# Kernel optimization log

Hardware: AMD Instinct MI355X
Metric: run time of the kernel (lower is better)

## Reference

```python
import jax, jax.numpy as jnp
import numpy as np

CHUNK_SIZE = 64
EPS = 1e-6


def setup_inputs() -> dict:
    key = jax.random.key(0)
    ks = jax.random.split(key, 5)
    B, NH, S, DH = 2, 16, 4096, 64
    return {
        "q": jax.random.normal(ks[0], (B, NH, S, DH), dtype=jnp.float32),
        "k": jax.random.normal(ks[1], (B, NH, S, DH), dtype=jnp.float32),
        "v": jax.random.normal(ks[2], (B, NH, S, DH), dtype=jnp.float32),
        "igate_preact": jax.random.normal(ks[3], (B, NH, S), dtype=jnp.float32),
        "fgate_preact": jax.random.normal(ks[4], (B, NH, S), dtype=jnp.float32),
    }


def _mlstm_intra(q, k, v, ig, fg, chunk_size, eps):
    # q,k,v: [B,NH,S,DH]; ig,fg: [B,NH,S]
    B, NH, S, DH = q.shape
    L = chunk_size
    NC = S // L
    qc = q.reshape(B, NH, NC, L, DH)
    kc = k.reshape(B, NH, NC, L, DH)
    vc = v.reshape(B, NH, NC, L, DH)
    igc = ig.reshape(B, NH, NC, L)
    fgc = fg.reshape(B, NH, NC, L)

    # log forget gates and their within-chunk cumulative sums
    log_fg = jax.nn.log_sigmoid(fgc)                      # [B,NH,NC,L]
    log_fg_cum = jnp.cumsum(log_fg, axis=-1)              # [B,NH,NC,L]

    # gated decay matrix: logD[i,j] = sum_{t=j+1..i} log f_t + i_j  for j<=i
    log_fg_mat = log_fg_cum[..., :, None] - log_fg_cum[..., None, :]  # [B,NH,NC,L,L]
    log_D = log_fg_mat + igc[..., None, :]
    causal = jnp.tril(jnp.ones((L, L), dtype=bool))
    log_D = jnp.where(causal, log_D, -jnp.inf)

    # stabilizer (row-wise max)
    m = jnp.max(log_D, axis=-1)                           # [B,NH,NC,L]
    D = jnp.exp(log_D - m[..., None])                     # [B,NH,NC,L,L]

    # QK scores scaled, gated by decay matrix
    scale = 1.0 / jnp.sqrt(jnp.asarray(DH, dtype=q.dtype))
    scores = jnp.einsum("bncld,bncsd->bncls", qc, kc) * scale
    C = scores * D                                        # [B,NH,NC,L,L]

    # stabilized normalizer: max(|row sum|, exp(-m))
    n = jnp.maximum(jnp.abs(jnp.sum(C, axis=-1)), jnp.exp(-m))  # [B,NH,NC,L]
    h = jnp.einsum("bncls,bncsd->bncld", C, vc) / (n[..., None] + eps)
    return h.reshape(B, NH, S, DH)


def reference(q, k, v, igate_preact, fgate_preact):
    return _mlstm_intra(q, k, v, igate_preact, fgate_preact, CHUNK_SIZE, EPS)
```

## Files before the change

### kernel.cpp

```cpp
#include <hip/hip_runtime.h>
#include <hip/hip_bf16.h>
#include <math.h>

namespace {

typedef __bf16 bf16x8 __attribute__((ext_vector_type(8)));
typedef float f32x4 __attribute__((ext_vector_type(4)));

constexpr int L = 64;
constexpr int DH = 64;

__device__ __forceinline__ int swz(int row, int col) {
  return row * 128 + (((col >> 3) ^ (row & 7)) << 4) + (col & 7) * 2;
}

__device__ __forceinline__ unsigned short bfbits(float f) {
  __bf16 h = (__bf16)f;
  return __builtin_bit_cast(unsigned short, h);
}
__device__ __forceinline__ __bf16 tobf(float f) { return (__bf16)f; }

__global__ __launch_bounds__(64) void mlstm_mfma(
    const float* __restrict__ q, const float* __restrict__ k,
    const float* __restrict__ v, const float* __restrict__ ig,
    const float* __restrict__ fg, float* __restrict__ out) {

  __shared__ __align__(16) char tile[64 * 128];
  __shared__ float ea_sh[64], eb_sh[64], em_sh[64];

  const int lane = threadIdx.x;
  const int m = lane & 15;
  const int g = lane >> 4;
  const size_t cbase = (size_t)blockIdx.x * (L * DH);
  const size_t gb = (size_t)blockIdx.x * L;

  const float fgv = fg[gb + lane];
  const float igv = ig[gb + lane];

  const float4* v4 = (const float4*)(v + cbase);
  float4 vbuf[16];
#pragma unroll
  for (int it = 0; it < 16; ++it) vbuf[it] = v4[it * 64 + lane];

  bf16x8 kf[4][2], qf[4][2];
#pragma unroll
  for (int rb = 0; rb < 4; ++rb)
#pragma unroll
    for (int kb = 0; kb < 2; ++kb) {
      const int off = (rb * 16 + m) * 64 + kb * 32 + g * 8;
      const float4 k0 = *(const float4*)(k + cbase + off);
      const float4 k1 = *(const float4*)(k + cbase + off + 4);
      const float4 q0 = *(const float4*)(q + cbase + off);
      const float4 q1 = *(const float4*)(q + cbase + off + 4);
      kf[rb][kb] = bf16x8{tobf(k0.x), tobf(k0.y), tobf(k0.z), tobf(k0.w),
                          tobf(k1.x), tobf(k1.y), tobf(k1.z), tobf(k1.w)};
      qf[rb][kb] = bf16x8{tobf(q0.x), tobf(q0.y), tobf(q0.z), tobf(q0.w),
                          tobf(q1.x), tobf(q1.y), tobf(q1.z), tobf(q1.w)};
    }

  {
    const float lf = fminf(fgv, 0.f) - log1pf(__expf(-fabsf(fgv)));
    float cum = lf;
#pragma unroll
    for (int o = 1; o < 64; o <<= 1) {
      const float t = __shfl_up(cum, o, 64);
      if (lane >= o) cum += t;
    }
    const float a = igv - cum;
    float b = a;
#pragma unroll
    for (int o = 1; o < 64; o <<= 1) {
      const float t = __shfl_up(b, o, 64);
      if (lane >= o) b = fmaxf(b, t);
    }
    const float bmax = __shfl(b, 63, 64);
    ea_sh[lane] = 0.125f * __expf(a - bmax);
    eb_sh[lane] = __expf(bmax - b);
    em_sh[lane] = __expf(-(b + cum));
  }

  {
    unsigned short* vt = (unsigned short*)tile;
#pragma unroll
    for (int it = 0; it < 16; ++it) {
      const int idx = it * 64 + lane;
      const int j = idx >> 4;
      const int d0 = (idx & 15) * 4;
      vt[swz(d0 + 0, j) >> 1] = bfbits(vbuf[it].x);
      vt[swz(d0 + 1, j) >> 1] = bfbits(vbuf[it].y);
      vt[swz(d0 + 2, j) >> 1] = bfbits(vbuf[it].z);
      vt[swz(d0 + 3, j) >> 1] = bfbits(vbuf[it].w);
    }
  }

  bf16x8 vfr[4][2];
#pragma unroll
  for (int db = 0; db < 4; ++db)
#pragma unroll
    for (int jb = 0; jb < 2; ++jb)
      vfr[db][jb] = *(const bf16x8*)(tile + swz(db * 16 + m, jb * 32 + g * 8));

  f32x4 st[4][4];
#pragma unroll
  for (int cb = 0; cb < 4; ++cb)
#pragma unroll
    for (int rb = 0; rb < 4; ++rb) {
      if (rb > cb) continue;
      f32x4 acc = {0.f, 0.f, 0.f, 0.f};
      acc = __builtin_amdgcn_mfma_f32_16x16x32_bf16(kf[rb][0], qf[cb][0], acc, 0, 0, 0);
      acc = __builtin_amdgcn_mfma_f32_16x16x32_bf16(kf[rb][1], qf[cb][1], acc, 0, 0, 0);
      st[rb][cb] = acc;
    }

  float ea_j[4][4];
#pragma unroll
  for (int rb = 0; rb < 4; ++rb)
#pragma unroll
    for (int e = 0; e < 4; ++e) ea_j[rb][e] = ea_sh[rb * 16 + g * 4 + e];

  float invr[4];
#pragma unroll
  for (int cb = 0; cb < 4; ++cb) {
    const int i = cb * 16 + m;
    const float ebv = eb_sh[i];
    float rs = 0.f;
#pragma unroll
    for (int rb = 0; rb < 4; ++rb) {
      unsigned long long wp = 0ull;
      if (rb <= cb) {
#pragma unroll
        for (int e = 0; e < 4; ++e) {
          const int j = rb * 16 + g * 4 + e;
          const float val = (j <= i) ? st[rb][cb][e] * ea_j[rb][e] * ebv : 0.f;
          rs += val;
          wp |= (unsigned long long)bfbits(val) << (16 * e);
        }
      }
      *(unsigned long long*)(tile + swz(i, rb * 16 + g * 4)) = wp;
    }
    rs += __shfl_xor(rs, 16, 64);
    rs += __shfl_xor(rs, 32, 64);
    const float n = fmaxf(fabsf(rs), em_sh[i]);
    invr[cb] = 1.f / (n + 1e-6f);
  }

#pragma unroll
  for (int ib = 0; ib < 4; ++ib) {
    const int i = ib * 16 + m;
    const bf16x8 c0 = *(const bf16x8*)(tile + swz(i, g * 8));
    f32x4 acc[4];
#pragma unroll
    for (int db = 0; db < 4; ++db) {
      f32x4 z = {0.f, 0.f, 0.f, 0.f};
      acc[db] = __builtin_amdgcn_mfma_f32_16x16x32_bf16(vfr[db][0], c0, z, 0, 0, 0);
    }
    if (ib >= 2) {
      const bf16x8 c1 = *(const bf16x8*)(tile + swz(i, 32 + g * 8));
#pragma unroll
      for (int db = 0; db < 4; ++db)
        acc[db] = __builtin_amdgcn_mfma_f32_16x16x32_bf16(vfr[db][1], c1, acc[db], 0, 0, 0);
    }
    const float iv = invr[ib];
    float* op = out + cbase + i * 64 + g * 4;
#pragma unroll
    for (int db = 0; db < 4; ++db) {
      const f32x4 hv = acc[db];
      *(float4*)(op + db * 16) =
          make_float4(hv[0] * iv, hv[1] * iv, hv[2] * iv, hv[3] * iv);
    }
  }
}

}

extern "C" void kernel_launch(void* const* d_in, const int* in_sizes, int n_in,
                              void* d_out, int out_size, void* d_ws,
                              size_t ws_size, hipStream_t stream) {
  const float* q = (const float*)d_in[0];
  const float* k = (const float*)d_in[1];
  const float* v = (const float*)d_in[2];
  const float* ig = (const float*)d_in[3];
  const float* fg = (const float*)d_in[4];
  float* out = (float*)d_out;

  const int total = in_sizes[0];
  const int nchunks = total / (L * DH);
  mlstm_mfma<<<dim3(nchunks), dim3(64), 0, stream>>>(q, k, v, ig, fg, out);
}
```

Measured before the change: 28.21 us.

## Split each chunk across four wavefronts, one per 16-row query block

Each chunk is now handled by a 256-thread block in which each wavefront owns one 16-row query block. It loads only the K blocks it needs under the causal mask and writes its C tile into a private LDS region. V is staged cooperatively, with a barrier so every wave can read the shared transposed V tile. The LDS swizzle key is also changed to reduce bank conflicts. The aim is more parallelism and latency hiding per chunk and shorter serial work per wave. The cost is a block-wide sync, some redundant K loads across waves, and load imbalance between the causal blocks.

```diff
diff --git a/kernel.cpp b/kernel.cpp
--- a/kernel.cpp
+++ b/kernel.cpp
@@ -10,8 +10,13 @@
 constexpr int L = 64;
 constexpr int DH = 64;
 
-__device__ __forceinline__ int swz(int row, int col) {
-  return row * 128 + (((col >> 3) ^ (row & 7)) << 4) + (col & 7) * 2;
+__device__ __forceinline__ int kkey(int r) { return (r ^ (r >> 2)) & 7; }
+
+__device__ __forceinline__ int swzV(int d, int j) {
+  return d * 128 + ((((j >> 3) ^ kkey(d)) & 7) << 4) + (j & 7) * 2;
+}
+__device__ __forceinline__ int swzC(int r, int j) {
+  return r * 128 + ((((j >> 3) ^ kkey(r)) & 7) << 4) + (j & 7) * 2;
 }
 
 __device__ __forceinline__ unsigned short bfbits(float f) {
@@ -20,45 +25,60 @@
 }
 __device__ __forceinline__ __bf16 tobf(float f) { return (__bf16)f; }
 
-__global__ __launch_bounds__(64) void mlstm_mfma(
+__global__ __launch_bounds__(256) void mlstm_mfma(
     const float* __restrict__ q, const float* __restrict__ k,
     const float* __restrict__ v, const float* __restrict__ ig,
     const float* __restrict__ fg, float* __restrict__ out) {
 
-  __shared__ __align__(16) char tile[64 * 128];
-  __shared__ float ea_sh[64], eb_sh[64], em_sh[64];
-
-  const int lane = threadIdx.x;
+  __shared__ __align__(16) char lds[8192 + 4 * 2048];
+  __shared__ __align__(16) float ea_sh[64];
+  __shared__ __align__(16) float eb_sh[64];
+  __shared__ __align__(16) float em_sh[64];
+
+  const int tid = threadIdx.x;
+  const int w = tid >> 6;
+  const int lane = tid & 63;
   const int m = lane & 15;
   const int g = lane >> 4;
   const size_t cbase = (size_t)blockIdx.x * (L * DH);
   const size_t gb = (size_t)blockIdx.x * L;
 
-  const float fgv = fg[gb + lane];
-  const float igv = ig[gb + lane];
-
   const float4* v4 = (const float4*)(v + cbase);
-  float4 vbuf[16];
-#pragma unroll
-  for (int it = 0; it < 16; ++it) vbuf[it] = v4[it * 64 + lane];
-
-  bf16x8 kf[4][2], qf[4][2];
-#pragma unroll
-  for (int rb = 0; rb < 4; ++rb)
-#pragma unroll
-    for (int kb = 0; kb < 2; ++kb) {
-      const int off = (rb * 16 + m) * 64 + kb * 32 + g * 8;
-      const float4 k0 = *(const float4*)(k + cbase + off);
-      const float4 k1 = *(const float4*)(k + cbase + off + 4);
-      const float4 q0 = *(const float4*)(q + cbase + off);
-      const float4 q1 = *(const float4*)(q + cbase + off + 4);
-      kf[rb][kb] = bf16x8{tobf(k0.x), tobf(k0.y), tobf(k0.z), tobf(k0.w),
-                          tobf(k1.x), tobf(k1.y), tobf(k1.z), tobf(k1.w)};
-      qf[rb][kb] = bf16x8{tobf(q0.x), tobf(q0.y), tobf(q0.z), tobf(q0.w),
-                          tobf(q1.x), tobf(q1.y), tobf(q1.z), tobf(q1.w)};
-    }
-
-  {
+  float4 vbuf[4];
+#pragma unroll
+  for (int it = 0; it < 4; ++it) vbuf[it] = v4[it * 256 + tid];
+
+  float fgv = 0.f, igv = 0.f;
+  if (w == 0) {
+    fgv = fg[gb + lane];
+    igv = ig[gb + lane];
+  }
+
+  bf16x8 qf[2];
+#pragma unroll
+  for (int kb = 0; kb < 2; ++kb) {
+    const int off = (w * 16 + m) * 64 + kb * 32 + g * 8;
+    const float4 q0 = *(const float4*)(q + cbase + off);
+    const float4 q1 = *(const float4*)(q + cbase + off + 4);
+    qf[kb] = bf16x8{tobf(q0.x), tobf(q0.y), tobf(q0.z), tobf(q0.w),
+                    tobf(q1.x), tobf(q1.y), tobf(q1.z), tobf(q1.w)};
+  }
+  bf16x8 kf[4][2];
+#pragma unroll
+  for (int rb = 0; rb < 4; ++rb) {
+    if (rb <= w) {
+#pragma unroll
+      for (int kb = 0; kb < 2; ++kb) {
+        const int off = (rb * 16 + m) * 64 + kb * 32 + g * 8;
+        const float4 k0 = *(const float4*)(k + cbase + off);
+        const float4 k1 = *(const float4*)(k + cbase + off + 4);
+        kf[rb][kb] = bf16x8{tobf(k0.x), tobf(k0.y), tobf(k0.z), tobf(k0.w),
+                            tobf(k1.x), tobf(k1.y), tobf(k1.z), tobf(k1.w)};
+      }
+    }
+  }
+
+  if (w == 0) {
     const float lf = fminf(fgv, 0.f) - log1pf(__expf(-fabsf(fgv)));
     float cum = lf;
 #pragma unroll
@@ -80,94 +100,89 @@
   }
 
   {
-    unsigned short* vt = (unsigned short*)tile;
-#pragma unroll
-    for (int it = 0; it < 16; ++it) {
-      const int idx = it * 64 + lane;
+    unsigned short* vt = (unsigned short*)lds;
+#pragma unroll
+    for (int it = 0; it < 4; ++it) {
+      const int idx = it * 256 + tid;
       const int j = idx >> 4;
       const int d0 = (idx & 15) * 4;
-      vt[swz(d0 + 0, j) >> 1] = bfbits(vbuf[it].x);
-      vt[swz(d0 + 1, j) >> 1] = bfbits(vbuf[it].y);
-      vt[swz(d0 + 2, j) >> 1] = bfbits(vbuf[it].z);
-      vt[swz(d0 + 3, j) >> 1] = bfbits(vbuf[it].w);
-    }
-  }
-
+      vt[swzV(d0 + 0, j) >> 1] = bfbits(vbuf[it].x);
+      vt[swzV(d0 + 1, j) >> 1] = bfbits(vbuf[it].y);
+      vt[swzV(d0 + 2, j) >> 1] = bfbits(vbuf[it].z);
+      vt[swzV(d0 + 3, j) >> 1] = bfbits(vbuf[it].w);
+    }
+  }
+
+  __syncthreads();
+
+  const int njb = (w >= 2) ? 2 : 1;
   bf16x8 vfr[4][2];
 #pragma unroll
   for (int db = 0; db < 4; ++db)
 #pragma unroll
     for (int jb = 0; jb < 2; ++jb)
-      vfr[db][jb] = *(const bf16x8*)(tile + swz(db * 16 + m, jb * 32 + g * 8));
-
-  f32x4 st[4][4];
-#pragma unroll
-  for (int cb = 0; cb < 4; ++cb)
-#pragma unroll
-    for (int rb = 0; rb < 4; ++rb) {
-      if (rb > cb) continue;
+      if (jb < njb)
+        vfr[db][jb] =
+            *(const bf16x8*)(lds + swzV(db * 16 + m, jb * 32 + g * 8));
+
+  f32x4 st[4];
+#pragma unroll
+  for (int rb = 0; rb < 4; ++rb) {
+    if (rb <= w) {
       f32x4 acc = {0.f, 0.f, 0.f, 0.f};
-      acc = __builtin_amdgcn_mfma_f32_16x16x32_bf16(kf[rb][0], qf[cb][0], acc, 0, 0, 0);
-      acc = __builtin_amdgcn_mfma_f32_16x16x32_bf16(kf[rb][1], qf[cb][1], acc, 0, 0, 0);
-      st[rb][cb] = acc;
-    }
-
-  float ea_j[4][4];
-#pragma unroll
-  for (int rb = 0; rb < 4; ++rb)
-#pragma unroll
-    for (int e = 0; e < 4; ++e) ea_j[rb][e] = ea_sh[rb * 16 + g * 4 + e];
-
-  float invr[4];
-#pragma unroll
-  for (int cb = 0; cb < 4; ++cb) {
-    const int i = cb * 16 + m;
-    const float ebv = eb_sh[i];
-    float rs = 0.f;
-#pragma unroll
-    for (int rb = 0; rb < 4; ++rb) {
+      acc = __builtin_amdgcn_mfma_f32_16x16x32_bf16(kf[rb][0], qf[0], acc, 0, 0, 0);
+      acc = __builtin_amdgcn_mfma_f32_16x16x32_bf16(kf[rb][1], qf[1], acc, 0, 0, 0);
+      st[rb] = acc;
+    }
+  }
+
+  char* cw = lds + 8192 + w * 2048;
+  const int i = w * 16 + m;
+  const float ebv = eb_sh[i];
+  float rs = 0.f;
+  const int rbfill = w | 1;
+#pragma unroll
+  for (int rb = 0; rb < 4; ++rb) {
+    if (rb <= rbfill) {
       unsigned long long wp = 0ull;
-      if (rb <= cb) {
+      if (rb <= w) {
+        const float4 ea4 = *(const float4*)&ea_sh[rb * 16 + g * 4];
+        const float eav[4] = {ea4.x, ea4.y, ea4.z, ea4.w};
 #pragma unroll
         for (int e = 0; e < 4; ++e) {
           const int j = rb * 16 + g * 4 + e;
-          const float val = (j <= i) ? st[rb][cb][e] * ea_j[rb][e] * ebv : 0.f;
+          const float val = (j <= i) ? st[rb][e] * eav[e] * ebv : 0.f;
           rs += val;
           wp |= (unsigned long long)bfbits(val) << (16 * e);
         }
       }
-      *(unsigned long long*)(tile + swz(i, rb * 16 + g * 4)) = wp;
-    }
-    rs += __shfl_xor(rs, 16, 64);
-    rs += __shfl_xor(rs, 32, 64);
-    const float n = fmaxf(fabsf(rs), em_sh[i]);
-    invr[cb] = 1.f / (n + 1e-6f);
-  }
-
-#pragma unroll
-  for (int ib = 0; ib < 4; ++ib) {
-    const int i = ib * 16 + m;
-    const bf16x8 c0 = *(const bf16x8*)(tile + swz(i, g * 8));
-    f32x4 acc[4];
-#pragma unroll
-    for (int db = 0; db < 4; ++db) {
-      f32x4 z = {0.f, 0.f, 0.f, 0.f};
-      acc[db] = __builtin_amdgcn_mfma_f32_16x16x32_bf16(vfr[db][0], c0, z, 0, 0, 0);
-    }
-    if (ib >= 2) {
-      const bf16x8 c1 = *(const bf16x8*)(tile + swz(i, 32 + g * 8));
-#pragma unroll
-      for (int db = 0; db < 4; ++db)
-        acc[db] = __builtin_amdgcn_mfma_f32_16x16x32_bf16(vfr[db][1], c1, acc[db], 0, 0, 0);
-    }
-    const float iv = invr[ib];
-    float* op = out + cbase + i * 64 + g * 4;
-#pragma unroll
-    for (int db = 0; db < 4; ++db) {
-      const f32x4 hv = acc[db];
-      *(float4*)(op + db * 16) =
-          make_float4(hv[0] * iv, hv[1] * iv, hv[2] * iv, hv[3] * iv);
-    }
+      *(unsigned long long*)(cw + swzC(m, rb * 16 + g * 4)) = wp;
+    }
+  }
+  rs += __shfl_xor(rs, 16, 64);
+  rs += __shfl_xor(rs, 32, 64);
+  const float invv = 1.f / (fmaxf(fabsf(rs), em_sh[i]) + 1e-6f);
+
+  const bf16x8 c0 = *(const bf16x8*)(cw + swzC(m, g * 8));
+  f32x4 acc[4];
+#pragma unroll
+  for (int db = 0; db < 4; ++db) {
+    f32x4 z = {0.f, 0.f, 0.f, 0.f};
+    acc[db] = __builtin_amdgcn_mfma_f32_16x16x32_bf16(vfr[db][0], c0, z, 0, 0, 0);
+  }
+  if (w >= 2) {
+    const bf16x8 c1 = *(const bf16x8*)(cw + swzC(m, 32 + g * 8));
+#pragma unroll
+    for (int db = 0; db < 4; ++db)
+      acc[db] = __builtin_amdgcn_mfma_f32_16x16x32_bf16(vfr[db][1], c1, acc[db], 0, 0, 0);
+  }
+
+  float* op = out + cbase + i * 64 + g * 4;
+#pragma unroll
+  for (int db = 0; db < 4; ++db) {
+    const f32x4 hv = acc[db];
+    *(float4*)(op + db * 16) =
+        make_float4(hv[0] * invv, hv[1] * invv, hv[2] * invv, hv[3] * invv);
   }
 }
 
@@ -185,5 +200,5 @@
 
   const int total = in_sizes[0];
   const int nchunks = total / (L * DH);
-  mlstm_mfma<<<dim3(nchunks), dim3(64), 0, stream>>>(q, k, v, ig, fg, out);
-}
+  mlstm_mfma<<<dim3(nchunks), dim3(256), 0, stream>>>(q, k, v, ig, fg, out);
+}
```

Measured after the change: 30.26 us. 7.3% more time.
